# Kernel optimization log

Measured on AMD Instinct MI355X. Metric: run time of the kernel, lower is better.

Reference implementation:

```python
import jax, jax.numpy as jnp
import numpy as np

N_NODES = 200000
N_GRAPHS = 1024
BN_EPS = 1e-5


def setup_inputs() -> dict:
    key = jax.random.key(0)
    ks = jax.random.split(key, 24)
    s = 0.05
    inp = {
        "x": jax.random.normal(ks[0], (N_NODES, 78), jnp.float32),
        "edge_index": jax.random.randint(ks[1], (2, 3200000), 0, N_NODES, jnp.int32),
        "batch": jnp.sort(jax.random.randint(ks[2], (N_NODES,), 0, N_GRAPHS, jnp.int32)),
        "target": jax.random.randint(ks[3], (N_GRAPHS, 1000), 0, 26, jnp.int32),
        "g1_w1": jax.random.normal(ks[4], (78, 32), jnp.float32) * s,
        "g1_b1": jnp.zeros((32,), jnp.float32),
        "g1_w2": jax.random.normal(ks[5], (32, 32), jnp.float32) * s,
        "g1_b2": jnp.zeros((32,), jnp.float32),
        "gW1": jax.random.normal(ks[6], (4, 32, 32), jnp.float32) * s,
        "gb1": jnp.zeros((4, 32), jnp.float32),
        "gW2": jax.random.normal(ks[7], (4, 32, 32), jnp.float32) * s,
        "gb2": jnp.zeros((4, 32), jnp.float32),
        "bn_gamma": jnp.ones((5, 32), jnp.float32),
        "bn_beta": jnp.zeros((5, 32), jnp.float32),
        "fcxd_w": jax.random.normal(ks[8], (32, 128), jnp.float32) * s,
        "fcxd_b": jnp.zeros((128,), jnp.float32),
        "embed_xt": jax.random.normal(ks[9], (26, 128), jnp.float32) * s,
        "conv_w": jax.random.normal(ks[10], (32, 1000, 8), jnp.float32) * 0.01,
        "conv_b": jnp.zeros((32,), jnp.float32),
        "fcxt_w": jax.random.normal(ks[11], (3872, 128), jnp.float32) * 0.01,
        "fcxt_b": jnp.zeros((128,), jnp.float32),
        "fc1_w": jax.random.normal(ks[12], (256, 1024), jnp.float32) * s,
        "fc1_b": jnp.zeros((1024,), jnp.float32),
        "fc2_w": jax.random.normal(ks[13], (1024, 256), jnp.float32) * s,
        "fc2_b": jnp.zeros((256,), jnp.float32),
        "out_w": jax.random.normal(ks[14], (256, 1), jnp.float32) * s,
        "out_b": jnp.zeros((1,), jnp.float32),
    }
    return inp


def _gin_layer(h, edge_index, W1, b1, W2, b2, gamma, beta):
    # GINConv (eps=0): mlp(x + sum_{j in N(i)} x_j), then ReLU then BatchNorm
    agg = jax.ops.segment_sum(h[edge_index[0]], edge_index[1], num_segments=N_NODES)
    z = h + agg
    z = jnp.maximum(z @ W1 + b1, 0.0) @ W2 + b2
    z = jnp.maximum(z, 0.0)
    mu = z.mean(axis=0)
    var = z.var(axis=0)
    return (z - mu) * jax.lax.rsqrt(var + BN_EPS) * gamma + beta


def reference(x, edge_index, batch, target,
              g1_w1, g1_b1, g1_w2, g1_b2,
              gW1, gb1, gW2, gb2, bn_gamma, bn_beta,
              fcxd_w, fcxd_b, embed_xt, conv_w, conv_b,
              fcxt_w, fcxt_b, fc1_w, fc1_b, fc2_w, fc2_b, out_w, out_b):
    # --- molecule GIN branch (dropout = identity at inference) ---
    h = _gin_layer(x, edge_index, g1_w1, g1_b1, g1_w2, g1_b2, bn_gamma[0], bn_beta[0])
    for i in range(4):
        h = _gin_layer(h, edge_index, gW1[i], gb1[i], gW2[i], gb2[i],
                       bn_gamma[i + 1], bn_beta[i + 1])
    # global add pool over graphs
    pooled = jax.ops.segment_sum(h, batch, num_segments=N_GRAPHS)  # [B,32]
    xd = jnp.maximum(pooled @ fcxd_w + fcxd_b, 0.0)                # [B,128]

    # --- protein branch: embed -> Conv1d(in_ch=seq_len=1000, k=8) -> linear ---
    e = embed_xt[target]                                            # [B,1000,128]
    conv = jax.lax.conv_general_dilated(
        e, conv_w, window_strides=(1,), padding='VALID',
        dimension_numbers=('NCH', 'OIH', 'NCH'))                    # [B,32,121]
    conv = conv + conv_b[None, :, None]
    xt = conv.reshape(conv.shape[0], -1) @ fcxt_w + fcxt_b          # [B,128]

    # --- combined dense head ---
    xc = jnp.concatenate([xd, xt], axis=1)                          # [B,256]
    xc = jnp.maximum(xc @ fc1_w + fc1_b, 0.0)
    xc = xc @ fc2_w + fc2_b
    return xc @ out_w + out_b                                       # [B,1]
```

## Files before the change

kernel.cpp:

```cpp
#include <hip/hip_runtime.h>
#include <hip/hip_fp16.h>

#define HID 32
#define BN_EPS 1e-5f
#define NBMAX 512
#define BSHIFT 9
#define SCAT_CH 8192
#define FSTRIDE 10240
#define FCAP 10240

static __device__ __forceinline__ int lbound(const int* a, int n, int key) {
    int lo = 0, hi = n;
    while (lo < hi) { int m = (lo + hi) >> 1; if (a[m] < key) lo = m + 1; else hi = m; }
    return lo;
}

static __device__ __forceinline__ unsigned packh2(float a, float b) {
    __half2 h = __floats2half2_rn(a, b);
    return *reinterpret_cast<unsigned*>(&h);
}
static __device__ __forceinline__ float lo_h(unsigned v) {
    __half2 h = *reinterpret_cast<__half2*>(&v);
    return __low2float(h);
}
static __device__ __forceinline__ float hi_h(unsigned v) {
    __half2 h = *reinterpret_cast<__half2*>(&v);
    return __high2float(h);
}
static __device__ __forceinline__ float h2f(unsigned short v) {
    return __half2float(__ushort_as_half(v));
}

static __device__ __forceinline__ void addu4h(float* a, uint4 v) {
    a[0] += lo_h(v.x); a[1] += hi_h(v.x);
    a[2] += lo_h(v.y); a[3] += hi_h(v.y);
    a[4] += lo_h(v.z); a[5] += hi_h(v.z);
    a[6] += lo_h(v.w); a[7] += hi_h(v.w);
}

__global__ void __launch_bounds__(256) k_bscatter(const int* __restrict__ ei,
                                                  int* __restrict__ gcur,
                                                  int* __restrict__ pairs, int E, int NB) {
    __shared__ int h[NBMAX];
    __shared__ int lb[NBMAX];
    int t = threadIdx.x;
    int c0 = blockIdx.x * SCAT_CH;
    int end = min(c0 + SCAT_CH, E);
    for (int i = t; i < NBMAX; i += 256) h[i] = 0;
    __syncthreads();
    for (int i = c0 + t; i < end; i += 256)
        atomicAdd(&h[ei[E + i] >> BSHIFT], 1);
    __syncthreads();
    for (int b = t; b < NB; b += 256) {
        int c = h[b];
        lb[b] = c ? atomicAdd(&gcur[b], c) : 0;
        h[b] = 0;
    }
    __syncthreads();
    for (int i = c0 + t; i < end; i += 256) {
        int src = ei[i], d = ei[E + i];
        int bkt = d >> BSHIFT;
        int r = atomicAdd(&h[bkt], 1);
        pairs[bkt * FSTRIDE + lb[bkt] + r] = src | ((d & 511) << 18);
    }
}

__global__ void __launch_bounds__(512) k_bscan(const int* __restrict__ gcur,
                                               int* __restrict__ bbase,
                                               int* __restrict__ rowstart,
                                               int N, int E, int NB) {
    __shared__ int s[512];
    int t = threadIdx.x;
    int v = (t < NB) ? gcur[t] : 0;
    s[t] = v; __syncthreads();
    for (int off = 1; off < 512; off <<= 1) {
        int u = (t >= off) ? s[t - off] : 0; __syncthreads();
        s[t] += u; __syncthreads();
    }
    int excl = s[t] - v;
    if (t < NB) bbase[t] = excl;
    if (t == NB - 1) bbase[NB] = s[t];
    if (t == 0) rowstart[N] = E;
}

__global__ void __launch_bounds__(512) k_bfinal(const int* __restrict__ pairs,
                                                const int* __restrict__ bbase,
                                                const int* __restrict__ gcur,
                                                int* __restrict__ rowstart,
                                                int* __restrict__ csr, int N) {
    __shared__ int h[2048];
    __shared__ int ts[512];
    __shared__ int loc[FCAP];
    int t = threadIdx.x;
    int b = blockIdx.x;
    int base = bbase[b];
    int cnt = gcur[b];
    const int* bp = pairs + (size_t)b * FSTRIDE;
    for (int i = t; i < 2048; i += 512) h[i] = 0;
    __syncthreads();
    for (int i = t; i < cnt; i += 512) {
        int p = bp[i];
        int key = ((p >> 18) << 2) | ((p & 0x3ffff) >> 16);
        atomicAdd(&h[key], 1);
    }
    __syncthreads();
    int v0 = h[4 * t], v1 = h[4 * t + 1], v2 = h[4 * t + 2], v3 = h[4 * t + 3];
    int lsum = v0 + v1 + v2 + v3;
    ts[t] = lsum; __syncthreads();
    for (int off = 1; off < 512; off <<= 1) {
        int u = (t >= off) ? ts[t - off] : 0; __syncthreads();
        ts[t] += u; __syncthreads();
    }
    int texcl = ts[t] - lsum;
    h[4 * t]     = texcl;
    h[4 * t + 1] = texcl + v0;
    h[4 * t + 2] = texcl + v0 + v1;
    h[4 * t + 3] = texcl + v0 + v1 + v2;
    int node = b * 512 + t;
    if (node < N) rowstart[node] = base + texcl;
    __syncthreads();
    bool fit = (cnt <= FCAP);
    for (int i = t; i < cnt; i += 512) {
        int p = bp[i];
        int key = ((p >> 18) << 2) | ((p & 0x3ffff) >> 16);
        int r = atomicAdd(&h[key], 1);
        int src = p & 0x3ffff;
        if (fit) loc[r] = src; else csr[base + r] = src;
    }
    __syncthreads();
    if (fit)
        for (int i = t; i < cnt; i += 512) csr[base + i] = loc[i];
}

__global__ void __launch_bounds__(256) k_A1(const float* __restrict__ x,
                                            const float* __restrict__ W,
                                            unsigned* __restrict__ Ub, int N) {
    __shared__ float xl[64 * 79];
    __shared__ float wl[78 * 33];
    int t = threadIdx.x;
    int n0 = blockIdx.x * 64;
    for (int idx = t; idx < 78 * 32; idx += 256)
        wl[(idx >> 5) * 33 + (idx & 31)] = W[idx];
    long base = (long)n0 * 78;
    for (int idx = t; idx < 64 * 78; idx += 256) {
        long g = base + idx;
        xl[(idx / 78) * 79 + (idx % 78)] = (g < (long)N * 78) ? x[g] : 0.f;
    }
    __syncthreads();
    int jp = t & 15, rg = t >> 4;
    for (int rep = 0; rep < 4; rep++) {
        int n = rg + 16 * rep;
        int node = n0 + n;
        if (node >= N) break;
        float a0 = 0.f, a1 = 0.f;
        #pragma unroll
        for (int k = 0; k < 78; k++) {
            float xv = xl[n * 79 + k];
            a0 += xv * wl[k * 33 + 2 * jp];
            a1 += xv * wl[k * 33 + 2 * jp + 1];
        }
        Ub[(size_t)node * 16 + jp] = packh2(a0, a1);
    }
}

__global__ void __launch_bounds__(256) k_BCS0(const uint4* __restrict__ Ub4,
                                              const int* __restrict__ rowstart,
                                              const int* __restrict__ csr,
                                              const float* __restrict__ b1,
                                              const float* __restrict__ W2,
                                              const float* __restrict__ b2,
                                              unsigned* __restrict__ Outb,
                                              float* __restrict__ slot, int N) {
    __shared__ float w2s[32 * 33];
    __shared__ float tl[64 * 33];
    __shared__ float redS[8][33];
    __shared__ float redQ[8][33];
    int t = threadIdx.x;
    for (int idx = t; idx < 1024; idx += 256)
        w2s[(idx >> 5) * 33 + (idx & 31)] = W2[idx];

    int g = t >> 2, l = t & 3;
    int node = blockIdx.x * 64 + g;
    bool act = (node < N);
    int s0 = 0, s1 = 0;
    if (act) { s0 = rowstart[node]; s1 = rowstart[node + 1]; }
    float a[8] = {0.f, 0.f, 0.f, 0.f, 0.f, 0.f, 0.f, 0.f};
    if (act) addu4h(a, Ub4[(size_t)node * 4 + l]);
    int e = s0;
    for (; e + 1 < s1; e += 2) {
        int sa = csr[e], sb = csr[e + 1];
        uint4 va = Ub4[(size_t)sa * 4 + l];
        uint4 vb = Ub4[(size_t)sb * 4 + l];
        addu4h(a, va);
        addu4h(a, vb);
    }
    if (e < s1) addu4h(a, Ub4[(size_t)csr[e] * 4 + l]);
    int f0 = 8 * l;
    #pragma unroll
    for (int i = 0; i < 8; i++)
        tl[g * 33 + f0 + i] = fmaxf(a[i] + b1[f0 + i], 0.f);
    __syncthreads();

    int j = t & 31, rg2 = t >> 5;
    float ps = 0.f, pq = 0.f;
    for (int rep = 0; rep < 8; rep++) {
        int n = rg2 + 8 * rep;
        int nod2 = blockIdx.x * 64 + n;
        float acc = b2[j];
        #pragma unroll
        for (int k = 0; k < 32; k++) acc += tl[n * 33 + k] * w2s[k * 33 + j];
        float xv = fmaxf(acc, 0.f);
        tl[n * 33 + j] = xv;
        if (nod2 < N) { ps += xv; pq += xv * xv; }
    }
    redS[rg2][j] = ps; redQ[rg2][j] = pq;
    __syncthreads();
    if (t < 32) {
        float s = 0.f, q = 0.f;
        #pragma unroll
        for (int r = 0; r < 8; r++) { s += redS[r][t]; q += redQ[r][t]; }
        int rep = blockIdx.x & 7;
        atomicAdd(&slot[rep * 64 + t], s);
        atomicAdd(&slot[rep * 64 + 32 + t], q);
    }
    for (int idx = t; idx < 1024; idx += 256) {
        int n = idx >> 4, jp = idx & 15;
        int nod = blockIdx.x * 64 + n;
        if (nod < N)
            Outb[(size_t)nod * 16 + jp] = packh2(tl[n * 33 + 2 * jp], tl[n * 33 + 2 * jp + 1]);
    }
}

__global__ void __launch_bounds__(256) k_BCS1(const uint4* __restrict__ Xb4,
                                              const int* __restrict__ rowstart,
                                              const int* __restrict__ csr,
                                              const float* __restrict__ pslot,
                                              const float* __restrict__ pgam,
                                              const float* __restrict__ pbet,
                                              const float* __restrict__ W1,
                                              const float* __restrict__ b1,
                                              const float* __restrict__ W2,
                                              const float* __restrict__ b2,
                                              unsigned* __restrict__ Outb,
                                              float* __restrict__ slot, int N) {
    __shared__ float w1s[32 * 33];
    __shared__ float w2s[32 * 33];
    __shared__ float zl[64 * 33];
    __shared__ float aa[32], cc[32], cw[32];
    __shared__ float dp1[64];
    __shared__ float redS[8][33];
    __shared__ float redQ[8][33];
    int t = threadIdx.x;
    if (t < 32) {
        float s = 0.f, q = 0.f;
        #pragma unroll
        for (int r = 0; r < 8; r++) { s += pslot[r * 64 + t]; q += pslot[r * 64 + 32 + t]; }
        float mu = s / (float)N;
        float var = q / (float)N - mu * mu;
        float av = pgam[t] * rsqrtf(var + BN_EPS);
        aa[t] = av;
        cc[t] = pbet[t] - mu * av;
    }
    __syncthreads();
    for (int idx = t; idx < 1024; idx += 256) {
        int k = idx >> 5, j = idx & 31;
        w1s[k * 33 + j] = aa[k] * W1[idx];
        w2s[k * 33 + j] = W2[idx];
    }
    if (t < 32) {
        float acc = 0.f;
        for (int k = 0; k < 32; k++) acc += cc[k] * W1[k * 32 + t];
        cw[t] = acc;
    }

    int g = t >> 2, l = t & 3;
    int node = blockIdx.x * 64 + g;
    bool act = (node < N);
    int s0 = 0, s1 = 0;
    if (act) { s0 = rowstart[node]; s1 = rowstart[node + 1]; }
    float a[8] = {0.f, 0.f, 0.f, 0.f, 0.f, 0.f, 0.f, 0.f};
    if (act) addu4h(a, Xb4[(size_t)node * 4 + l]);
    int e = s0;
    for (; e + 1 < s1; e += 2) {
        int sa = csr[e], sb = csr[e + 1];
        uint4 va = Xb4[(size_t)sa * 4 + l];
        uint4 vb = Xb4[(size_t)sb * 4 + l];
        addu4h(a, va);
        addu4h(a, vb);
    }
    if (e < s1) addu4h(a, Xb4[(size_t)csr[e] * 4 + l]);
    int f0 = 8 * l;
    #pragma unroll
    for (int i = 0; i < 8; i++) zl[g * 33 + f0 + i] = a[i];
    if (l == 0) dp1[g] = (float)(s1 - s0 + 1);
    __syncthreads();

    int j = t & 31, rg2 = t >> 5;
    float ps = 0.f, pq = 0.f;
    for (int rep = 0; rep < 8; rep++) {
        int n = rg2 + 8 * rep;
        float acc = dp1[n] * cw[j] + b1[j];
        #pragma unroll
        for (int k = 0; k < 32; k++) acc += zl[n * 33 + k] * w1s[k * 33 + j];
        zl[n * 33 + j] = fmaxf(acc, 0.f);
        float o = b2[j];
        #pragma unroll
        for (int k = 0; k < 32; k++) o += zl[n * 33 + k] * w2s[k * 33 + j];
        float xv = fmaxf(o, 0.f);
        zl[n * 33 + j] = xv;
        int nod2 = blockIdx.x * 64 + n;
        if (nod2 < N) { ps += xv; pq += xv * xv; }
    }
    redS[rg2][j] = ps; redQ[rg2][j] = pq;
    __syncthreads();
    if (t < 32) {
        float s = 0.f, q = 0.f;
        #pragma unroll
        for (int r = 0; r < 8; r++) { s += redS[r][t]; q += redQ[r][t]; }
        int rep = blockIdx.x & 7;
        atomicAdd(&slot[rep * 64 + t], s);
        atomicAdd(&slot[rep * 64 + 32 + t], q);
    }
    for (int idx = t; idx < 1024; idx += 256) {
        int n = idx >> 4, jp = idx & 15;
        int nod = blockIdx.x * 64 + n;
        if (nod < N)
            Outb[(size_t)nod * 16 + jp] = packh2(zl[n * 33 + 2 * jp], zl[n * 33 + 2 * jp + 1]);
    }
}

__global__ void __launch_bounds__(128) k_pool(const unsigned short* __restrict__ Xb,
                                              const int* __restrict__ batch,
                                              const float* __restrict__ pslot,
                                              const float* __restrict__ pgam,
                                              const float* __restrict__ pbet,
                                              const float* __restrict__ fw,
                                              const float* __restrict__ fb,
                                              float* __restrict__ xc, int N) {
    __shared__ float red[4][32];
    __shared__ float pv[32];
    __shared__ float aa[32], cc[32];
    int g = blockIdx.x, t = threadIdx.x;
    if (t < 32) {
        float s = 0.f, q = 0.f;
        #pragma unroll
        for (int r = 0; r < 8; r++) { s += pslot[r * 64 + t]; q += pslot[r * 64 + 32 + t]; }
        float mu = s / (float)N;
        float var = q / (float)N - mu * mu;
        float av = pgam[t] * rsqrtf(var + BN_EPS);
        aa[t] = av;
        cc[t] = pbet[t] - mu * av;
    }
    int lo = lbound(batch, N, g);
    int hi = lbound(batch, N, g + 1);
    int j = t & 31, rs = t >> 5;
    float ps = 0.f;
    for (int i = lo + rs; i < hi; i += 4) ps += h2f(Xb[(size_t)i * 32 + j]);
    red[rs][j] = ps; __syncthreads();
    if (t < 32) {
        float s = red[0][t] + red[1][t] + red[2][t] + red[3][t];
        pv[t] = s * aa[t] + (float)(hi - lo) * cc[t];
    }
    __syncthreads();
    float acc = fb[t];
    for (int k = 0; k < 32; k++) acc += pv[k] * fw[k * 128 + t];
    xc[g * 256 + t] = fmaxf(acc, 0.f);
}

__global__ void __launch_bounds__(128) k_F2(const float* __restrict__ Emb,
                                            const float* __restrict__ fcxt,
                                            float* __restrict__ F) {
    __shared__ float er[128];
    int bid = blockIdx.x;
    int v = bid >> 5, o = bid & 31;
    int t = threadIdx.x;
    er[t] = Emb[v * 128 + t];
    __syncthreads();
    float acc[8] = {0.f, 0.f, 0.f, 0.f, 0.f, 0.f, 0.f, 0.f};
    for (int p = 0; p < 121; p++) {
        float fv = fcxt[(o * 121 + p) * 128 + t];
        #pragma unroll
        for (int k = 0; k < 8; k++) acc[k] += er[p + k] * fv;
    }
    #pragma unroll
    for (int k = 0; k < 8; k++)
        F[((size_t)v * 256 + o * 8 + k) * 128 + t] = acc[k];
}

__global__ void __launch_bounds__(128) k_cb(const float* __restrict__ fcxt,
                                            const float* __restrict__ fb,
                                            const float* __restrict__ cb,
                                            float* __restrict__ cbias) {
    int o = blockIdx.x, t = threadIdx.x;
    float acc = 0.f;
    for (int p = 0; p < 121; p++) acc += fcxt[(o * 121 + p) * 128 + t];
    float val = cb[o] * acc;
    if (o == 0) val += fb[t];
    atomicAdd(&cbias[t], val);
}

__global__ void __launch_bounds__(256) k_D2(const float* __restrict__ cw,
                                            const float* __restrict__ F,
                                            unsigned* __restrict__ Dmb) {
    __shared__ float Fl[32][128];
    __shared__ float Wl[32][64];
    int v = blockIdx.y;
    int c0 = blockIdx.x * 64;
    int t = threadIdx.x;
    int jg = t & 31, j0 = jg * 4;
    int cg = t >> 5;
    float4 acc[8];
    #pragma unroll
    for (int i = 0; i < 8; i++) acc[i] = make_float4(0.f, 0.f, 0.f, 0.f);
    for (int chunk = 0; chunk < 8; chunk++) {
        int k0 = chunk * 32;
        __syncthreads();
        for (int idx = t; idx < 4096; idx += 256) {
            int k = idx >> 7, j = idx & 127;
            Fl[k][j] = F[((size_t)v * 256 + k0 + k) * 128 + j];
        }
        for (int idx = t; idx < 2048; idx += 256) {
            int k = idx >> 6, c = idx & 63;
            int ok = k0 + k;
            Wl[k][c] = (c0 + c < 1000) ? cw[((ok >> 3) * 1000 + c0 + c) * 8 + (ok & 7)] : 0.f;
        }
        __syncthreads();
        for (int k = 0; k < 32; k++) {
            float4 fv = *(const float4*)&Fl[k][j0];
            #pragma unroll
            for (int ci = 0; ci < 8; ci++) {
                float wv = Wl[k][cg * 8 + ci];
                acc[ci].x += wv * fv.x;
                acc[ci].y += wv * fv.y;
                acc[ci].z += wv * fv.z;
                acc[ci].w += wv * fv.w;
            }
        }
    }
    #pragma unroll
    for (int ci = 0; ci < 8; ci++) {
        int c = c0 + cg * 8 + ci;
        if (c < 1000) {
            uint2 pk;
            pk.x = packh2(acc[ci].x, acc[ci].y);
            pk.y = packh2(acc[ci].z, acc[ci].w);
            *(uint2*)&Dmb[((size_t)c * 26 + v) * 64 + jg * 2] = pk;
        }
    }
}

__global__ void __launch_bounds__(256) k_xt3(const int* __restrict__ target,
                                             const uint4* __restrict__ Dm4,
                                             const float* __restrict__ cbias,
                                             float* __restrict__ xc) {
    __shared__ int tl[1000];
    __shared__ float red[16][132];
    int b = blockIdx.x, t = threadIdx.x;
    for (int i = t; i < 1000; i += 256) tl[i] = target[(size_t)b * 1000 + i];
    __syncthreads();
    int cl = t >> 4;
    int jg = t & 15;
    float acc[8] = {0.f, 0.f, 0.f, 0.f, 0.f, 0.f, 0.f, 0.f};
    for (int c = cl; c < 1000; c += 16) {
        int v = tl[c];
        uint4 d = Dm4[((size_t)c * 26 + v) * 16 + jg];
        acc[0] += lo_h(d.x); acc[1] += hi_h(d.x);
        acc[2] += lo_h(d.y); acc[3] += hi_h(d.y);
        acc[4] += lo_h(d.z); acc[5] += hi_h(d.z);
        acc[6] += lo_h(d.w); acc[7] += hi_h(d.w);
    }
    #pragma unroll
    for (int fi = 0; fi < 8; fi++) red[cl][jg * 8 + fi] = acc[fi];
    __syncthreads();
    if (t < 128) {
        float s = 0.f;
        #pragma unroll
        for (int r = 0; r < 16; r++) s += red[r][t];
        xc[(size_t)b * 256 + 128 + t] = cbias[t] + s;
    }
}

__global__ void __launch_bounds__(256) k_fc1(const float* __restrict__ xc,
                                             const float* __restrict__ w,
                                             const float* __restrict__ bias,
                                             float* __restrict__ y1) {
    __shared__ float xl[16 * 256];
    int t = threadIdx.x;
    int q0 = blockIdx.x * 256, b0 = blockIdx.y * 16;
    for (int idx = t; idx < 4096; idx += 256) xl[idx] = xc[b0 * 256 + idx];
    __syncthreads();
    int ql = t & 63, q = q0 + ql * 4;
    int bg = t >> 6;
    float4 bv = *(const float4*)&bias[q];
    float4 acc0 = bv, acc1 = bv, acc2 = bv, acc3 = bv;
    const float* xr = &xl[bg * 4 * 256];
    #pragma unroll 4
    for (int k = 0; k < 256; k++) {
        float4 wv = *(const float4*)&w[k * 1024 + q];
        float x0 = xr[k], x1 = xr[256 + k], x2 = xr[512 + k], x3 = xr[768 + k];
        acc0.x += x0 * wv.x; acc0.y += x0 * wv.y; acc0.z += x0 * wv.z; acc0.w += x0 * wv.w;
        acc1.x += x1 * wv.x; acc1.y += x1 * wv.y; acc1.z += x1 * wv.z; acc1.w += x1 * wv.w;
        acc2.x += x2 * wv.x; acc2.y += x2 * wv.y; acc2.z += x2 * wv.z; acc2.w += x2 * wv.w;
        acc3.x += x3 * wv.x; acc3.y += x3 * wv.y; acc3.z += x3 * wv.z; acc3.w += x3 * wv.w;
    }
    int b = b0 + bg * 4;
    float4 r;
    r.x = fmaxf(acc0.x, 0.f); r.y = fmaxf(acc0.y, 0.f); r.z = fmaxf(acc0.z, 0.f); r.w = fmaxf(acc0.w, 0.f);
    *(float4*)&y1[(size_t)b * 1024 + q] = r;
    r.x = fmaxf(acc1.x, 0.f); r.y = fmaxf(acc1.y, 0.f); r.z = fmaxf(acc1.z, 0.f); r.w = fmaxf(acc1.w, 0.f);
    *(float4*)&y1[(size_t)(b + 1) * 1024 + q] = r;
    r.x = fmaxf(acc2.x, 0.f); r.y = fmaxf(acc2.y, 0.f); r.z = fmaxf(acc2.z, 0.f); r.w = fmaxf(acc2.w, 0.f);
    *(float4*)&y1[(size_t)(b + 2) * 1024 + q] = r;
    r.x = fmaxf(acc3.x, 0.f); r.y = fmaxf(acc3.y, 0.f); r.z = fmaxf(acc3.z, 0.f); r.w = fmaxf(acc3.w, 0.f);
    *(float4*)&y1[(size_t)(b + 3) * 1024 + q] = r;
}

__global__ void k_wcomb(const float* __restrict__ fc2w, const float* __restrict__ fc2b,
                        const float* __restrict__ ow, const float* __restrict__ ob,
                        float* __restrict__ wc) {
    int p = blockIdx.x * 256 + threadIdx.x;
    float acc = 0.f;
    for (int q = 0; q < 256; q++) acc += fc2w[p * 256 + q] * ow[q];
    wc[p] = acc;
    if (p == 0) {
        float bc = ob[0];
        for (int q = 0; q < 256; q++) bc += fc2b[q] * ow[q];
        wc[1024] = bc;
    }
}

__global__ void __launch_bounds__(256) k_out(const float* __restrict__ y1,
                                             const float* __restrict__ wc,
                                             float* __restrict__ out) {
    __shared__ float r[256];
    int b = blockIdx.x, t = threadIdx.x;
    float acc = 0.f;
    for (int p = t; p < 1024; p += 256) acc += y1[b * 1024 + p] * wc[p];
    r[t] = acc; __syncthreads();
    for (int off = 128; off > 0; off >>= 1) {
        if (t < off) r[t] += r[t + off];
        __syncthreads();
    }
    if (t == 0) out[b] = r[0] + wc[1024];
}

extern "C" void kernel_launch(void* const* d_in, const int* in_sizes, int n_in,
                              void* d_out, int out_size, void* d_ws, size_t ws_size,
                              hipStream_t stream) {
    const float* x     = (const float*)d_in[0];
    const int*   ei    = (const int*)d_in[1];
    const int*   batch = (const int*)d_in[2];
    const int*   targ  = (const int*)d_in[3];
    const float* g1w1  = (const float*)d_in[4];
    const float* g1b1  = (const float*)d_in[5];
    const float* g1w2  = (const float*)d_in[6];
    const float* g1b2  = (const float*)d_in[7];
    const float* gW1   = (const float*)d_in[8];
    const float* gb1   = (const float*)d_in[9];
    const float* gW2   = (const float*)d_in[10];
    const float* gb2   = (const float*)d_in[11];
    const float* gam   = (const float*)d_in[12];
    const float* bet   = (const float*)d_in[13];
    const float* fcxdw = (const float*)d_in[14];
    const float* fcxdb = (const float*)d_in[15];
    const float* emb   = (const float*)d_in[16];
    const float* convw = (const float*)d_in[17];
    const float* convb = (const float*)d_in[18];
    const float* fcxtw = (const float*)d_in[19];
    const float* fcxtb = (const float*)d_in[20];
    const float* fc1w  = (const float*)d_in[21];
    const float* fc1b  = (const float*)d_in[22];
    const float* fc2w  = (const float*)d_in[23];
    const float* fc2b  = (const float*)d_in[24];
    const float* outw  = (const float*)d_in[25];
    const float* outb  = (const float*)d_in[26];

    int N = in_sizes[2];
    int E = in_sizes[1] / 2;
    int B = in_sizes[3] / 1000;
    int NB = (N + 511) >> BSHIFT;

    char* ws = (char*)d_ws;
    size_t off = 0;
    auto alloc = [&](size_t bytes) -> void* {
        void* p = ws + off;
        off += (bytes + 255) & ~(size_t)255;
        return p;
    };
    int*   rowstart = (int*)alloc((size_t)(N + 1) * 4);
    int*   bbase    = (int*)alloc((NBMAX + 1) * 4);
    int*   gcur     = (int*)alloc(NBMAX * 4);
    int*   csr      = (int*)alloc((size_t)E * 4);
    size_t xb_bytes = (size_t)N * 64;
    size_t pairs_bytes = (size_t)NB * FSTRIDE * 4;
    char*  blk      = (char*)alloc(2 * xb_bytes > pairs_bytes ? 2 * xb_bytes : pairs_bytes);
    unsigned* XbA   = (unsigned*)blk;
    unsigned* XbB   = (unsigned*)(blk + xb_bytes);
    int*   pairs    = (int*)blk;
    unsigned* Ub    = (unsigned*)alloc((size_t)N * 16 * 4);
    float* stats    = (float*)alloc((size_t)5 * 640 * 4);
    float* xc       = (float*)alloc((size_t)B * 256 * 4);
    float* Fb       = (float*)alloc((size_t)26 * 256 * 128 * 4);
    unsigned* Dmb   = (unsigned*)alloc((size_t)1000 * 26 * 64 * 4);
    float* cbias    = (float*)alloc(128 * 4);
    float* y1       = (float*)alloc((size_t)B * 1024 * 4);
    float* wc       = (float*)alloc(1025 * 4);

    hipMemsetAsync(gcur, 0, NBMAX * 4, stream);
    hipMemsetAsync(stats, 0, (size_t)5 * 640 * 4, stream);
    hipMemsetAsync(cbias, 0, 128 * 4, stream);

    k_bscatter<<<(E + SCAT_CH - 1) / SCAT_CH, 256, 0, stream>>>(ei, gcur, pairs, E, NB);
    k_bscan<<<1, 512, 0, stream>>>(gcur, bbase, rowstart, N, E, NB);
    k_bfinal<<<NB, 512, 0, stream>>>(pairs, bbase, gcur, rowstart, csr, N);

    int gBCS = (N + 63) / 64;

    k_A1<<<(N + 63) / 64, 256, 0, stream>>>(x, g1w1, Ub, N);
    k_BCS0<<<gBCS, 256, 0, stream>>>((const uint4*)Ub, rowstart, csr,
                                     g1b1, g1w2, g1b2, XbA, stats, N);

    unsigned* bufs[2] = {XbA, XbB};
    for (int i = 0; i < 4; i++) {
        unsigned* src = bufs[i & 1];
        unsigned* dst = bufs[(i + 1) & 1];
        k_BCS1<<<gBCS, 256, 0, stream>>>((const uint4*)src, rowstart, csr,
                                         stats + (size_t)i * 640, gam + i * 32, bet + i * 32,
                                         gW1 + i * 1024, gb1 + i * 32,
                                         gW2 + i * 1024, gb2 + i * 32,
                                         dst, stats + (size_t)(i + 1) * 640, N);
    }

    k_pool<<<B, 128, 0, stream>>>((const unsigned short*)XbA, batch,
                                  stats + (size_t)4 * 640, gam + 128, bet + 128,
                                  fcxdw, fcxdb, xc, N);

    k_F2<<<26 * 32, 128, 0, stream>>>(emb, fcxtw, Fb);
    k_cb<<<32, 128, 0, stream>>>(fcxtw, fcxtb, convb, cbias);
    dim3 gD(16, 26);
    k_D2<<<gD, 256, 0, stream>>>(convw, Fb, Dmb);
    k_xt3<<<B, 256, 0, stream>>>(targ, (const uint4*)Dmb, cbias, xc);

    dim3 g1(4, B / 16);
    k_fc1<<<g1, 256, 0, stream>>>(xc, fc1w, fc1b, y1);
    k_wcomb<<<4, 256, 0, stream>>>(fc2w, fc2b, outw, outb, wc);
    k_out<<<B, 256, 0, stream>>>(y1, wc, (float*)d_out);
}
```

Measured before the change: 666.1 us.

## Sort nodes by in-degree for load-balanced gather in GIN layers

Adds a counting sort of nodes by in-degree, built from a histogram, a descending scan and an atomic placement pass. The five GIN aggregation kernels then process nodes through this permutation, so each wavefront's 16 nodes have similar edge counts and less lane divergence. The neighbour gather loop is also unrolled from 2 to 4 loads for more memory-level parallelism. The cost is three extra kernel launches, one more indirection, and output writes scattered across nodes instead of contiguous.

```diff
diff --git a/kernel.cpp b/kernel.cpp
--- a/kernel.cpp
+++ b/kernel.cpp
@@ -132,6 +132,44 @@
         for (int i = t; i < cnt; i += 512) csr[base + i] = loc[i];
 }
 
+__global__ void __launch_bounds__(256) k_dhist(const int* __restrict__ rowstart,
+                                               int* __restrict__ dh, int N) {
+    __shared__ int h[512];
+    int t = threadIdx.x;
+    for (int i = t; i < 512; i += 256) h[i] = 0;
+    __syncthreads();
+    for (int i = blockIdx.x * 256 + t; i < N; i += gridDim.x * 256) {
+        int d = min(rowstart[i + 1] - rowstart[i], 511);
+        atomicAdd(&h[d], 1);
+    }
+    __syncthreads();
+    for (int i = t; i < 512; i += 256)
+        if (h[i]) atomicAdd(&dh[i], h[i]);
+}
+
+__global__ void __launch_bounds__(512) k_dscan(const int* __restrict__ dh,
+                                               int* __restrict__ dcur) {
+    __shared__ int s[512];
+    int t = threadIdx.x;
+    int v = dh[511 - t];
+    s[t] = v; __syncthreads();
+    for (int off = 1; off < 512; off <<= 1) {
+        int u = (t >= off) ? s[t - off] : 0; __syncthreads();
+        s[t] += u; __syncthreads();
+    }
+    dcur[511 - t] = s[t] - v;
+}
+
+__global__ void __launch_bounds__(256) k_dplace(const int* __restrict__ rowstart,
+                                                int* __restrict__ dcur,
+                                                int* __restrict__ perm, int N) {
+    for (int i = blockIdx.x * 256 + threadIdx.x; i < N; i += gridDim.x * 256) {
+        int d = min(rowstart[i + 1] - rowstart[i], 511);
+        int pos = atomicAdd(&dcur[d], 1);
+        perm[pos] = i;
+    }
+}
+
 __global__ void __launch_bounds__(256) k_A1(const float* __restrict__ x,
                                             const float* __restrict__ W,
                                             unsigned* __restrict__ Ub, int N) {
@@ -166,6 +204,7 @@
 __global__ void __launch_bounds__(256) k_BCS0(const uint4* __restrict__ Ub4,
                                               const int* __restrict__ rowstart,
                                               const int* __restrict__ csr,
+                                              const int* __restrict__ perm,
                                               const float* __restrict__ b1,
                                               const float* __restrict__ W2,
                                               const float* __restrict__ b2,
@@ -175,26 +214,33 @@
     __shared__ float tl[64 * 33];
     __shared__ float redS[8][33];
     __shared__ float redQ[8][33];
+    __shared__ int pl[64];
     int t = threadIdx.x;
     for (int idx = t; idx < 1024; idx += 256)
         w2s[(idx >> 5) * 33 + (idx & 31)] = W2[idx];
+    if (t < 64) {
+        int gid = blockIdx.x * 64 + t;
+        pl[t] = (gid < N) ? perm[gid] : -1;
+    }
+    __syncthreads();
 
     int g = t >> 2, l = t & 3;
-    int node = blockIdx.x * 64 + g;
-    bool act = (node < N);
+    int node = pl[g];
+    bool act = (node >= 0);
     int s0 = 0, s1 = 0;
     if (act) { s0 = rowstart[node]; s1 = rowstart[node + 1]; }
     float a[8] = {0.f, 0.f, 0.f, 0.f, 0.f, 0.f, 0.f, 0.f};
     if (act) addu4h(a, Ub4[(size_t)node * 4 + l]);
     int e = s0;
-    for (; e + 1 < s1; e += 2) {
-        int sa = csr[e], sb = csr[e + 1];
+    for (; e + 3 < s1; e += 4) {
+        int sa = csr[e], sb = csr[e + 1], sc = csr[e + 2], sd = csr[e + 3];
         uint4 va = Ub4[(size_t)sa * 4 + l];
         uint4 vb = Ub4[(size_t)sb * 4 + l];
-        addu4h(a, va);
-        addu4h(a, vb);
-    }
-    if (e < s1) addu4h(a, Ub4[(size_t)csr[e] * 4 + l]);
+        uint4 vc = Ub4[(size_t)sc * 4 + l];
+        uint4 vd = Ub4[(size_t)sd * 4 + l];
+        addu4h(a, va); addu4h(a, vb); addu4h(a, vc); addu4h(a, vd);
+    }
+    for (; e < s1; e++) addu4h(a, Ub4[(size_t)csr[e] * 4 + l]);
     int f0 = 8 * l;
     #pragma unroll
     for (int i = 0; i < 8; i++)
@@ -205,13 +251,12 @@
     float ps = 0.f, pq = 0.f;
     for (int rep = 0; rep < 8; rep++) {
         int n = rg2 + 8 * rep;
-        int nod2 = blockIdx.x * 64 + n;
         float acc = b2[j];
         #pragma unroll
         for (int k = 0; k < 32; k++) acc += tl[n * 33 + k] * w2s[k * 33 + j];
         float xv = fmaxf(acc, 0.f);
         tl[n * 33 + j] = xv;
-        if (nod2 < N) { ps += xv; pq += xv * xv; }
+        if (pl[n] >= 0) { ps += xv; pq += xv * xv; }
     }
     redS[rg2][j] = ps; redQ[rg2][j] = pq;
     __syncthreads();
@@ -225,8 +270,8 @@
     }
     for (int idx = t; idx < 1024; idx += 256) {
         int n = idx >> 4, jp = idx & 15;
-        int nod = blockIdx.x * 64 + n;
-        if (nod < N)
+        int nod = pl[n];
+        if (nod >= 0)
             Outb[(size_t)nod * 16 + jp] = packh2(tl[n * 33 + 2 * jp], tl[n * 33 + 2 * jp + 1]);
     }
 }
@@ -234,6 +279,7 @@
 __global__ void __launch_bounds__(256) k_BCS1(const uint4* __restrict__ Xb4,
                                               const int* __restrict__ rowstart,
                                               const int* __restrict__ csr,
+                                              const int* __restrict__ perm,
                                               const float* __restrict__ pslot,
                                               const float* __restrict__ pgam,
                                               const float* __restrict__ pbet,
@@ -250,6 +296,7 @@
     __shared__ float dp1[64];
     __shared__ float redS[8][33];
     __shared__ float redQ[8][33];
+    __shared__ int pl[64];
     int t = threadIdx.x;
     if (t < 32) {
         float s = 0.f, q = 0.f;
@@ -261,6 +308,10 @@
         aa[t] = av;
         cc[t] = pbet[t] - mu * av;
     }
+    if (t >= 64 && t < 128) {
+        int gid = blockIdx.x * 64 + (t - 64);
+        pl[t - 64] = (gid < N) ? perm[gid] : -1;
+    }
     __syncthreads();
     for (int idx = t; idx < 1024; idx += 256) {
         int k = idx >> 5, j = idx & 31;
@@ -274,21 +325,22 @@
     }
 
     int g = t >> 2, l = t & 3;
-    int node = blockIdx.x * 64 + g;
-    bool act = (node < N);
+    int node = pl[g];
+    bool act = (node >= 0);
     int s0 = 0, s1 = 0;
     if (act) { s0 = rowstart[node]; s1 = rowstart[node + 1]; }
     float a[8] = {0.f, 0.f, 0.f, 0.f, 0.f, 0.f, 0.f, 0.f};
     if (act) addu4h(a, Xb4[(size_t)node * 4 + l]);
     int e = s0;
-    for (; e + 1 < s1; e += 2) {
-        int sa = csr[e], sb = csr[e + 1];
+    for (; e + 3 < s1; e += 4) {
+        int sa = csr[e], sb = csr[e + 1], sc = csr[e + 2], sd = csr[e + 3];
         uint4 va = Xb4[(size_t)sa * 4 + l];
         uint4 vb = Xb4[(size_t)sb * 4 + l];
-        addu4h(a, va);
-        addu4h(a, vb);
-    }
-    if (e < s1) addu4h(a, Xb4[(size_t)csr[e] * 4 + l]);
+        uint4 vc = Xb4[(size_t)sc * 4 + l];
+        uint4 vd = Xb4[(size_t)sd * 4 + l];
+        addu4h(a, va); addu4h(a, vb); addu4h(a, vc); addu4h(a, vd);
+    }
+    for (; e < s1; e++) addu4h(a, Xb4[(size_t)csr[e] * 4 + l]);
     int f0 = 8 * l;
     #pragma unroll
     for (int i = 0; i < 8; i++) zl[g * 33 + f0 + i] = a[i];
@@ -308,8 +360,7 @@
         for (int k = 0; k < 32; k++) o += zl[n * 33 + k] * w2s[k * 33 + j];
         float xv = fmaxf(o, 0.f);
         zl[n * 33 + j] = xv;
-        int nod2 = blockIdx.x * 64 + n;
-        if (nod2 < N) { ps += xv; pq += xv * xv; }
+        if (pl[n] >= 0) { ps += xv; pq += xv * xv; }
     }
     redS[rg2][j] = ps; redQ[rg2][j] = pq;
     __syncthreads();
@@ -323,8 +374,8 @@
     }
     for (int idx = t; idx < 1024; idx += 256) {
         int n = idx >> 4, jp = idx & 15;
-        int nod = blockIdx.x * 64 + n;
-        if (nod < N)
+        int nod = pl[n];
+        if (nod >= 0)
             Outb[(size_t)nod * 16 + jp] = packh2(zl[n * 33 + 2 * jp], zl[n * 33 + 2 * jp + 1]);
     }
 }
@@ -591,6 +642,9 @@
     int*   bbase    = (int*)alloc((NBMAX + 1) * 4);
     int*   gcur     = (int*)alloc(NBMAX * 4);
     int*   csr      = (int*)alloc((size_t)E * 4);
+    int*   perm     = (int*)alloc((size_t)N * 4);
+    int*   dh       = (int*)alloc(512 * 4);
+    int*   dcur     = (int*)alloc(512 * 4);
     size_t xb_bytes = (size_t)N * 64;
     size_t pairs_bytes = (size_t)NB * FSTRIDE * 4;
     char*  blk      = (char*)alloc(2 * xb_bytes > pairs_bytes ? 2 * xb_bytes : pairs_bytes);
@@ -607,6 +661,7 @@
     float* wc       = (float*)alloc(1025 * 4);
 
     hipMemsetAsync(gcur, 0, NBMAX * 4, stream);
+    hipMemsetAsync(dh, 0, 512 * 4, stream);
     hipMemsetAsync(stats, 0, (size_t)5 * 640 * 4, stream);
     hipMemsetAsync(cbias, 0, 128 * 4, stream);
 
@@ -614,17 +669,21 @@
     k_bscan<<<1, 512, 0, stream>>>(gcur, bbase, rowstart, N, E, NB);
     k_bfinal<<<NB, 512, 0, stream>>>(pairs, bbase, gcur, rowstart, csr, N);
 
+    k_dhist<<<256, 256, 0, stream>>>(rowstart, dh, N);
+    k_dscan<<<1, 512, 0, stream>>>(dh, dcur);
+    k_dplace<<<256, 256, 0, stream>>>(rowstart, dcur, perm, N);
+
     int gBCS = (N + 63) / 64;
 
     k_A1<<<(N + 63) / 64, 256, 0, stream>>>(x, g1w1, Ub, N);
-    k_BCS0<<<gBCS, 256, 0, stream>>>((const uint4*)Ub, rowstart, csr,
+    k_BCS0<<<gBCS, 256, 0, stream>>>((const uint4*)Ub, rowstart, csr, perm,
                                      g1b1, g1w2, g1b2, XbA, stats, N);
 
     unsigned* bufs[2] = {XbA, XbB};
     for (int i = 0; i < 4; i++) {
         unsigned* src = bufs[i & 1];
         unsigned* dst = bufs[(i + 1) & 1];
-        k_BCS1<<<gBCS, 256, 0, stream>>>((const uint4*)src, rowstart, csr,
+        k_BCS1<<<gBCS, 256, 0, stream>>>((const uint4*)src, rowstart, csr, perm,
                                          stats + (size_t)i * 640, gam + i * 32, bet + i * 32,
                                          gW1 + i * 1024, gb1 + i * 32,
                                          gW2 + i * 1024, gb2 + i * 32,
```

Result: slower. 1.179 ms (+77.0%).
